# Kernel optimization log

Measured on AMD Instinct MI355X. Metric: run time of the kernel, lower is better.

Reference implementation:

```python
import jax, jax.numpy as jnp
import numpy as np

HEADS = 8
GROUPS = 32   # Group_cnt in the source
WIN = 16      # config.local_window_size


def _gn_nc(x, groups, eps):
    # group_norm on [N, C] (affine=False)
    N, C = x.shape
    xg = x.reshape(N, groups, C // groups)
    m = xg.mean(axis=2, keepdims=True)
    v = xg.var(axis=2, keepdims=True)
    return ((xg - m) / jnp.sqrt(v + eps)).reshape(N, C)


def _gn_nchw(x, groups, eps):
    # group_norm on [B, C, H, W] (affine=False)
    B, C, H, W = x.shape
    xg = x.reshape(B, groups, C // groups, H, W)
    m = xg.mean(axis=(2, 3, 4), keepdims=True)
    v = xg.var(axis=(2, 3, 4), keepdims=True)
    return ((xg - m) / jnp.sqrt(v + eps)).reshape(B, C, H, W)


def _conv3x3(x, w, b=None):
    y = jax.lax.conv_general_dilated(x, w, (1, 1), 'SAME',
                                     dimension_numbers=('NCHW', 'OIHW', 'NCHW'))
    return y if b is None else y + b[None, :, None, None]


def _forward(x, temb, conv1_w, conv1_b, conv2_w, g_diff, g_res, g2, g3,
             qkv2_w, qkv2_b, out2_w, qkv3_w, qkv3_b, out3_w,
             lsa_qkv_w, lsa_out_w):
    # ---- Residual_Block (layer1) ----
    h = _gn_nchw(x, GROUPS, 1e-6)
    h = _conv3x3(h, conv1_w, conv1_b)
    h = h + g_diff * temb[:, :, None, None]      # gate_diffusion (ReZero-style gate)
    h = jax.nn.silu(h)
    h = _gn_nchw(h, GROUPS, 1e-6)
    h = _conv3x3(h, conv2_w)
    h = _gn_nchw(h, GROUPS, 1e-6)
    x = x + g_res * h                            # gate_residual

    B, C, Fq, T = x.shape
    Dh = C // HEADS
    scale = 1.0 / jnp.sqrt(jnp.float32(Dh))      # (F/heads)**0.5 divisor

    # ---- SelfAttention over frequency axis (layer2): batch B*T, seq Fq ----
    xf = x.transpose(0, 3, 2, 1).reshape(B * T, Fq, C)
    qkv = xf @ qkv2_w + qkv2_b                   # [B*T, Fq, 3C]
    q, k, v = [t.reshape(B * T, Fq, HEADS, Dh) for t in jnp.split(qkv, 3, axis=-1)]
    p = jax.nn.softmax(jnp.einsum('bLhf,blhf->bLlh', q, k) * scale, axis=2)
    y = jnp.einsum('blhf,bLlh->bLhf', v, p).reshape(B * T, Fq, C) @ out2_w
    y = _gn_nc(y.reshape(-1, C), GROUPS, 1e-5).reshape(B * T, Fq, C)
    xf = xf + g2 * y                             # gate2

    # ---- GlobalAttention over time axis (layer3): batch B*Fq, seq T ----
    xt = xf.reshape(B, T, Fq, C).transpose(0, 2, 1, 3).reshape(B * Fq, T, C)
    qkv = xt @ qkv3_w + qkv3_b
    q, k, v = [t.reshape(B * Fq, T, HEADS, Dh) for t in jnp.split(qkv, 3, axis=-1)]
    p = jax.nn.softmax(jnp.einsum('bhf,blhf->blh', q.mean(axis=1), k) * scale, axis=1)
    y = jnp.einsum('blhf,blh->bhf', v, p).reshape(B * Fq, C) @ out3_w
    y = _gn_nc(y, GROUPS, 1e-5).reshape(B * Fq, 1, C)
    xt = xt + g3 * y                             # gate3, broadcast over T
    x = xt.reshape(B, Fq, T, C).transpose(0, 3, 1, 2)

    # ---- LSA_block (layer4): pre-norm local windowed attention along T, residual ----
    h = _gn_nchw(x, GROUPS, 1e-5)
    h = h.transpose(0, 2, 3, 1).reshape(B * Fq, T, C)
    nw = T // WIN
    qkv = (h @ lsa_qkv_w).reshape(B * Fq, nw, WIN, 3 * C)
    q, k, v = [t.reshape(B * Fq, nw, WIN, HEADS, Dh) for t in jnp.split(qkv, 3, axis=-1)]
    p = jax.nn.softmax(jnp.einsum('nwqhd,nwkhd->nwqkh', q, k) * scale, axis=3)
    o = jnp.einsum('nwqkh,nwkhd->nwqhd', p, v).reshape(B * Fq, T, C) @ lsa_out_w
    return x + o.reshape(B, Fq, T, C).transpose(0, 3, 1, 2)


def setup_inputs() -> dict:
    key = jax.random.key(0)
    ks = jax.random.split(key, 10)
    B, C, Fq, T = 4, 256, 64, 256
    w = lambda k, s: jax.random.normal(k, s, dtype=jnp.float32) * 0.02
    return {
        'x': jax.random.normal(ks[0], (B, C, Fq, T), dtype=jnp.float32),
        'temb': jax.random.normal(ks[1], (B, C), dtype=jnp.float32),
        'conv1_w': w(ks[2], (C, C, 3, 3)),
        'conv1_b': jnp.zeros((C,), jnp.float32),
        'conv2_w': w(ks[3], (C, C, 3, 3)),
        'g_diff': jnp.full((1,), 0.5, jnp.float32),
        'g_res': jnp.full((1,), 0.5, jnp.float32),
        'g2': jnp.full((1,), 0.5, jnp.float32),
        'g3': jnp.full((1,), 0.5, jnp.float32),
        'qkv2_w': w(ks[4], (C, 3 * C)),
        'qkv2_b': jnp.zeros((3 * C,), jnp.float32),
        'out2_w': w(ks[5], (C, C)),
        'qkv3_w': w(ks[6], (C, 3 * C)),
        'qkv3_b': jnp.zeros((3 * C,), jnp.float32),
        'out3_w': w(ks[7], (C, C)),
        'lsa_qkv_w': w(ks[8], (C, 3 * C)),
        'lsa_out_w': w(ks[9], (C, C)),
    }


def reference(x, temb, conv1_w, conv1_b, conv2_w, g_diff, g_res, g2, g3,
              qkv2_w, qkv2_b, out2_w, qkv3_w, qkv3_b, out3_w,
              lsa_qkv_w, lsa_out_w):
    return _forward(x, temb, conv1_w, conv1_b, conv2_w, g_diff, g_res, g2, g3,
                    qkv2_w, qkv2_b, out2_w, qkv3_w, qkv3_b, out3_w,
                    lsa_qkv_w, lsa_out_w)
```

## Files before the change

### kernel.cpp

```cpp
#include <hip/hip_runtime.h>

#define NN 16777216
#define CC 256
#define FF 64
#define TT 256

typedef short v8s __attribute__((ext_vector_type(8)));
typedef float v4f __attribute__((ext_vector_type(4)));

__device__ __forceinline__ unsigned short f2bf(float f) {
  unsigned u = __float_as_uint(f);
  u += 0x7fff + ((u >> 16) & 1);
  return (unsigned short)(u >> 16);
}
__device__ __forceinline__ float bf2f(unsigned short h) {
  return __uint_as_float(((unsigned)h) << 16);
}
__device__ __forceinline__ unsigned packbf2(float a, float b) {
  return (unsigned)f2bf(a) | ((unsigned)f2bf(b) << 16);
}
__device__ __forceinline__ void unpack8(uint4 u, float* d) {
  d[0] = __uint_as_float(u.x << 16); d[1] = __uint_as_float(u.x & 0xffff0000u);
  d[2] = __uint_as_float(u.y << 16); d[3] = __uint_as_float(u.y & 0xffff0000u);
  d[4] = __uint_as_float(u.z << 16); d[5] = __uint_as_float(u.z & 0xffff0000u);
  d[6] = __uint_as_float(u.w << 16); d[7] = __uint_as_float(u.w & 0xffff0000u);
}

__device__ __forceinline__ void blockReduce2(float& a, float& b, float* sbuf) {
  #pragma unroll
  for (int off = 32; off > 0; off >>= 1) {
    a += __shfl_down(a, off, 64);
    b += __shfl_down(b, off, 64);
  }
  int w = threadIdx.x >> 6;
  if ((threadIdx.x & 63) == 0) { sbuf[w] = a; sbuf[4 + w] = b; }
  __syncthreads();
  if (threadIdx.x == 0) {
    a = sbuf[0] + sbuf[1] + sbuf[2] + sbuf[3];
    b = sbuf[4] + sbuf[5] + sbuf[6] + sbuf[7];
  }
}

__global__ void prep_all_k(const float* __restrict__ c1w, const float* __restrict__ c2w,
    const float* __restrict__ q2w, const float* __restrict__ o2w, const float* __restrict__ q3w,
    const float* __restrict__ lqw, const float* __restrict__ low,
    unsigned short* __restrict__ WB1, unsigned short* __restrict__ WB2,
    unsigned short* __restrict__ Q2T, unsigned short* __restrict__ O2T,
    unsigned short* __restrict__ Q3T, unsigned short* __restrict__ LQT,
    unsigned short* __restrict__ LOT, float* __restrict__ stats) {
  long s = (long)blockIdx.x * 256 + threadIdx.x;
  if (s < 1024) { stats[s] = 0.f; return; }
  s -= 1024;
  if (s < 589824) {
    int co = (int)(s / 2304), r = (int)(s % 2304);
    int ci = r / 9, tap = r % 9;
    WB1[(tap * 256 + co) * 256 + ci] = f2bf(c1w[s]);
    return;
  }
  s -= 589824;
  if (s < 589824) {
    int co = (int)(s / 2304), r = (int)(s % 2304);
    int ci = r / 9, tap = r % 9;
    WB2[(tap * 256 + co) * 256 + ci] = f2bf(c2w[s]);
    return;
  }
  s -= 589824;
  if (s < 196608) { int k = (int)(s / 768), n = (int)(s % 768); Q2T[n * 256 + k] = f2bf(q2w[s]); return; }
  s -= 196608;
  if (s < 65536)  { int k = (int)(s / 256), n = (int)(s % 256); O2T[n * 256 + k] = f2bf(o2w[s]); return; }
  s -= 65536;
  if (s < 196608) { int k = (int)(s / 768), n = (int)(s % 768); Q3T[n * 256 + k] = f2bf(q3w[s]); return; }
  s -= 196608;
  if (s < 196608) { int k = (int)(s / 768), n = (int)(s % 768); LQT[n * 256 + k] = f2bf(lqw[s]); return; }
  s -= 196608;
  if (s < 65536)  { int k = (int)(s / 256), n = (int)(s % 256); LOT[n * 256 + k] = f2bf(low[s]); return; }
}

__global__ __launch_bounds__(256) void gn_stats_contig(const float* __restrict__ src, float* __restrict__ stats) {
  __shared__ float sbuf[8];
  int grp = blockIdx.x >> 3, chunk = blockIdx.x & 7;
  const float4* p = (const float4*)src + grp * 32768 + chunk * 4096;
  float s = 0.f, ss = 0.f;
  for (int i = threadIdx.x; i < 4096; i += 256) {
    float4 v = p[i];
    s += v.x + v.y + v.z + v.w;
    ss += v.x * v.x + v.y * v.y + v.z * v.z + v.w * v.w;
  }
  blockReduce2(s, ss, sbuf);
  if (threadIdx.x == 0) { atomicAdd(&stats[grp], s); atomicAdd(&stats[128 + grp], ss); }
}

__global__ __launch_bounds__(256) void gn_apply_tr_k(const float* __restrict__ src,
    const float* __restrict__ stats, unsigned short* __restrict__ XC, float eps) {
  __shared__ float sT[32][33];
  int bx = blockIdx.x;
  int r = bx >> 6;
  int c0 = ((bx >> 3) & 7) * 32;
  int t0 = (bx & 7) * 32;
  int b = r >> 6, f = r & 63;
  int tl = threadIdx.x & 31, tr = threadIdx.x >> 5;
  #pragma unroll
  for (int i = 0; i < 4; ++i) {
    int c = c0 + tr + i * 8;
    int grp = b * 32 + (c >> 3);
    float mean = stats[grp] * (1.f / 131072.f);
    float var = stats[128 + grp] * (1.f / 131072.f) - mean * mean;
    float rv = rsqrtf(var + eps);
    float v = src[((b * 256 + c) * 64 + f) * 256 + t0 + tl];
    sT[tr + i * 8][tl] = (v - mean) * rv;
  }
  __syncthreads();
  #pragma unroll
  for (int i = 0; i < 4; ++i) {
    int t = t0 + tr + i * 8;
    XC[(((size_t)(b * 64 + f)) * 256 + t) * 256 + c0 + tl] = f2bf(sT[tl][tr + i * 8]);
  }
}

__global__ __launch_bounds__(256) void gn_tr_resid_k(const float* __restrict__ h,
    const float* __restrict__ x, const float* __restrict__ stats,
    const float* __restrict__ gate, float* __restrict__ XF, float eps) {
  __shared__ float sT[32][33];
  int bx = blockIdx.x;
  int r = bx >> 6;
  int c0 = ((bx >> 3) & 7) * 32;
  int t0 = (bx & 7) * 32;
  int b = r >> 6, f = r & 63;
  int tl = threadIdx.x & 31, tr = threadIdx.x >> 5;
  float g = gate[0];
  #pragma unroll
  for (int i = 0; i < 4; ++i) {
    int c = c0 + tr + i * 8;
    int grp = b * 32 + (c >> 3);
    float mean = stats[grp] * (1.f / 131072.f);
    float var = stats[128 + grp] * (1.f / 131072.f) - mean * mean;
    float rv = rsqrtf(var + eps);
    int idx = ((b * 256 + c) * 64 + f) * 256 + t0 + tl;
    sT[tr + i * 8][tl] = x[idx] + g * (h[idx] - mean) * rv;
  }
  __syncthreads();
  #pragma unroll
  for (int i = 0; i < 4; ++i) {
    int t = t0 + tr + i * 8;
    XF[(((size_t)(b * 256 + t)) * 64 + f) * 256 + c0 + tl] = sT[tl][tr + i * 8];
  }
}

__global__ __launch_bounds__(256, 4) void conv3x3_mfma_k(const unsigned short* __restrict__ XC,
    const unsigned short* __restrict__ wb, const float* __restrict__ bias,
    const float* __restrict__ temb, const float* __restrict__ gd,
    float* __restrict__ out, float* __restrict__ ostats, int mode) {
  __shared__ __align__(16) unsigned short sIn[258][40];
  __shared__ __align__(16) unsigned short sW[3][64][40];
  int f  = blockIdx.x;
  int b  = blockIdx.y >> 2;
  int co0 = (blockIdx.y & 3) * 64;
  int tid = threadIdx.x;
  int wave = tid >> 6, lane = tid & 63;
  int lm = lane & 15, quad = lane >> 4;
  int w64 = wave * 64;
  v4f acc[4][4];
  #pragma unroll
  for (int i = 0; i < 4; ++i)
    #pragma unroll
    for (int j = 0; j < 4; ++j) acc[i][j] = (v4f)(0.f);

  for (int ci0 = 0; ci0 < 256; ci0 += 32) {
    for (int df = 0; df < 3; ++df) {
      __syncthreads();
      for (int s = tid; s < 1032; s += 256) {
        int tl = s >> 2, part = s & 3;
        int fi = f + df - 1, tg = tl - 1;
        uint4 val = make_uint4(0, 0, 0, 0);
        if (fi >= 0 && fi < 64 && tg >= 0 && tg < 256)
          val = *(const uint4*)&XC[(((size_t)(b * 64 + fi)) * 256 + tg) * 256 + ci0 + part * 8];
        *(uint4*)&sIn[tl][part * 8] = val;
      }
      for (int s = tid; s < 768; s += 256) {
        int tap3 = s >> 8, r = s & 255;
        int co = r >> 2, part = r & 3;
        *(uint4*)&sW[tap3][co][part * 8] =
            *(const uint4*)&wb[((size_t)((df * 3 + tap3) * 256) + co0 + co) * 256 + ci0 + part * 8];
      }
      __syncthreads();
      #pragma unroll
      for (int dt = 0; dt < 3; ++dt) {
        v8s A[4];
        #pragma unroll
        for (int mt = 0; mt < 4; ++mt)
          A[mt] = *(const v8s*)&sIn[w64 + mt * 16 + lm + dt][quad * 8];
        #pragma unroll
        for (int nt = 0; nt < 4; ++nt) {
          v8s B = *(const v8s*)&sW[dt][nt * 16 + lm][quad * 8];
          #pragma unroll
          for (int mt = 0; mt < 4; ++mt)
            acc[mt][nt] = __builtin_amdgcn_mfma_f32_16x16x32_bf16(A[mt], B, acc[mt][nt], 0, 0, 0);
        }
      }
    }
  }
  __syncthreads();
  float* sStat = (float*)sIn;
  float gdv = mode ? gd[0] : 0.f;
  float sch, qch;
  #pragma unroll
  for (int nt = 0; nt < 4; ++nt) {
    int co = co0 + nt * 16 + lm;
    float bb = 0.f;
    if (mode) bb = bias[co] + gdv * temb[b * 256 + co];
    sch = 0.f; qch = 0.f;
    #pragma unroll
    for (int mt = 0; mt < 4; ++mt) {
      int t = w64 + mt * 16 + quad * 4;
      float v0 = acc[mt][nt][0] + bb, v1 = acc[mt][nt][1] + bb;
      float v2 = acc[mt][nt][2] + bb, v3 = acc[mt][nt][3] + bb;
      if (mode) {
        v0 = v0 / (1.f + expf(-v0)); v1 = v1 / (1.f + expf(-v1));
        v2 = v2 / (1.f + expf(-v2)); v3 = v3 / (1.f + expf(-v3));
      }
      float4 o; o.x = v0; o.y = v1; o.z = v2; o.w = v3;
      *(float4*)&out[(((size_t)b * 256 + co) * 64 + f) * 256 + t] = o;
      sch += v0 + v1 + v2 + v3;
      qch += v0 * v0 + v1 * v1 + v2 * v2 + v3 * v3;
    }
    sch += __shfl_xor(sch, 16); qch += __shfl_xor(qch, 16);
    sch += __shfl_xor(sch, 32); qch += __shfl_xor(qch, 32);
    if (quad == 0) {
      sStat[((wave * 4 + nt) * 16 + lm) * 2]     = sch;
      sStat[((wave * 4 + nt) * 16 + lm) * 2 + 1] = qch;
    }
  }
  __syncthreads();
  if (tid < 64) {
    int c = tid;
    int nt = c >> 4, lmm = c & 15;
    float s = 0.f, q = 0.f;
    #pragma unroll
    for (int w = 0; w < 4; ++w) {
      s += sStat[((w * 4 + nt) * 16 + lmm) * 2];
      q += sStat[((w * 4 + nt) * 16 + lmm) * 2 + 1];
    }
    s += __shfl_xor(s, 1); q += __shfl_xor(q, 1);
    s += __shfl_xor(s, 2); q += __shfl_xor(q, 2);
    s += __shfl_xor(s, 4); q += __shfl_xor(q, 4);
    if ((c & 7) == 0) {
      int g = (co0 + c) >> 3;
      atomicAdd(&ostats[b * 32 + g], s);
      atomicAdd(&ostats[128 + b * 32 + g], q);
    }
  }
}

__global__ __launch_bounds__(256) void gemm_af32_k(const float* __restrict__ A, int lda,
    const unsigned short* __restrict__ BT, const float* __restrict__ bias,
    unsigned short* __restrict__ Cb, int ldc,
    const float* __restrict__ gstats, int growbase, float eps) {
  __shared__ __align__(16) unsigned short sA[128][40];
  __shared__ __align__(16) unsigned short sB[128][40];
  int n0 = blockIdx.x * 128, m0 = blockIdx.y * 128;
  int tid = threadIdx.x;
  int wave = tid >> 6, lane = tid & 63;
  int wm = wave >> 1, wn = wave & 1;
  int lm = lane & 15, quad = lane >> 4;
  v4f acc[4][4];
  #pragma unroll
  for (int i = 0; i < 4; ++i)
    #pragma unroll
    for (int j = 0; j < 4; ++j) acc[i][j] = (v4f)(0.f);

  for (int k0 = 0; k0 < 256; k0 += 32) {
    __syncthreads();
    #pragma unroll
    for (int i = 0; i < 4; ++i) {
      int s = tid + i * 256;
      int row = s >> 3, k4 = s & 7;
      float4 av = *(const float4*)&A[(size_t)(m0 + row) * lda + k0 + k4 * 4];
      if (gstats) {
        int grp = ((growbase + m0 + row) >> 14) * 32 + ((k0 + k4 * 4) >> 3);
        float mean = gstats[grp] * (1.f / 131072.f);
        float var = gstats[128 + grp] * (1.f / 131072.f) - mean * mean;
        float rr = rsqrtf(var + eps);
        av.x = (av.x - mean) * rr; av.y = (av.y - mean) * rr;
        av.z = (av.z - mean) * rr; av.w = (av.w - mean) * rr;
      }
      *(uint2*)&sA[row][k4 * 4] = make_uint2(packbf2(av.x, av.y), packbf2(av.z, av.w));
    }
    #pragma unroll
    for (int i = 0; i < 2; ++i) {
      int s = tid + i * 256;
      int n = s >> 2, part = s & 3;
      *(uint4*)&sB[n][part * 8] = *(const uint4*)&BT[(size_t)(n0 + n) * 256 + k0 + part * 8];
    }
    __syncthreads();
    v8s Af[4];
    #pragma unroll
    for (int mt = 0; mt < 4; ++mt)
      Af[mt] = *(const v8s*)&sA[wm * 64 + mt * 16 + lm][quad * 8];
    #pragma unroll
    for (int nt = 0; nt < 4; ++nt) {
      v8s Bf = *(const v8s*)&sB[wn * 64 + nt * 16 + lm][quad * 8];
      #pragma unroll
      for (int mt = 0; mt < 4; ++mt)
        acc[mt][nt] = __builtin_amdgcn_mfma_f32_16x16x32_bf16(Af[mt], Bf, acc[mt][nt], 0, 0, 0);
    }
  }
  #pragma unroll
  for (int nt = 0; nt < 4; ++nt) {
    int col = n0 + wn * 64 + nt * 16 + lm;
    float bb = bias ? bias[col] : 0.f;
    #pragma unroll
    for (int mt = 0; mt < 4; ++mt) {
      int row = m0 + wm * 64 + mt * 16 + quad * 4;
      #pragma unroll
      for (int r = 0; r < 4; ++r)
        Cb[(size_t)(row + r) * ldc + col] = f2bf(acc[mt][nt][r] + bb);
    }
  }
}

__global__ __launch_bounds__(256) void gemm_abf16_k(const unsigned short* __restrict__ A, int lda,
    const unsigned short* __restrict__ BT, float* __restrict__ xf,
    unsigned short* __restrict__ Cb, int ldc, const float* __restrict__ gate) {
  __shared__ __align__(16) unsigned short sA[128][40];
  __shared__ __align__(16) unsigned short sB[128][40];
  int n0 = blockIdx.x * 128, m0 = blockIdx.y * 128;
  int tid = threadIdx.x;
  int wave = tid >> 6, lane = tid & 63;
  int wm = wave >> 1, wn = wave & 1;
  int lm = lane & 15, quad = lane >> 4;
  v4f acc[4][4];
  #pragma unroll
  for (int i = 0; i < 4; ++i)
    #pragma unroll
    for (int j = 0; j < 4; ++j) acc[i][j] = (v4f)(0.f);

  for (int k0 = 0; k0 < 256; k0 += 32) {
    __syncthreads();
    #pragma unroll
    for (int i = 0; i < 2; ++i) {
      int s = tid + i * 256;
      int row = s >> 2, part = s & 3;
      *(uint4*)&sA[row][part * 8] = *(const uint4*)&A[(size_t)(m0 + row) * lda + k0 + part * 8];
      *(uint4*)&sB[row][part * 8] = *(const uint4*)&BT[(size_t)(n0 + row) * 256 + k0 + part * 8];
    }
    __syncthreads();
    v8s Af[4];
    #pragma unroll
    for (int mt = 0; mt < 4; ++mt)
      Af[mt] = *(const v8s*)&sA[wm * 64 + mt * 16 + lm][quad * 8];
    #pragma unroll
    for (int nt = 0; nt < 4; ++nt) {
      v8s Bf = *(const v8s*)&sB[wn * 64 + nt * 16 + lm][quad * 8];
      #pragma unroll
      for (int mt = 0; mt < 4; ++mt)
        acc[mt][nt] = __builtin_amdgcn_mfma_f32_16x16x32_bf16(Af[mt], Bf, acc[mt][nt], 0, 0, 0);
    }
  }
  if (xf) {
    float g = gate[0];
    #pragma unroll
    for (int mt = 0; mt < 4; ++mt) {
      int rowb = m0 + wm * 64 + mt * 16 + quad * 4;
      #pragma unroll
      for (int r = 0; r < 4; ++r) {
        #pragma unroll
        for (int nt = 0; nt < 4; ++nt) {
          float v = acc[mt][nt][r];
          float s = v, q = v * v;
          s += __shfl_xor(s, 1); q += __shfl_xor(q, 1);
          s += __shfl_xor(s, 2); q += __shfl_xor(q, 2);
          s += __shfl_xor(s, 4); q += __shfl_xor(q, 4);
          float m = s * 0.125f;
          float var = q * 0.125f - m * m;
          float norm = (v - m) * rsqrtf(var + 1e-5f);
          int col = n0 + wn * 64 + nt * 16 + lm;
          size_t idx = (size_t)(rowb + r) * 256 + col;
          xf[idx] += g * norm;
        }
      }
    }
  } else {
    #pragma unroll
    for (int nt = 0; nt < 4; ++nt) {
      int col = n0 + wn * 64 + nt * 16 + lm;
      #pragma unroll
      for (int mt = 0; mt < 4; ++mt) {
        int row = m0 + wm * 64 + mt * 16 + quad * 4;
        #pragma unroll
        for (int r = 0; r < 4; ++r)
          Cb[(size_t)(row + r) * ldc + col] = f2bf(acc[mt][nt][r]);
      }
    }
  }
}

__global__ __launch_bounds__(256) void gemm_k(const float* __restrict__ A, int lda,
    const float* __restrict__ Bm, int N, const float* __restrict__ bias,
    float* __restrict__ Cm, int ldc) {
  __shared__ __align__(16) float sA[16][64];
  __shared__ __align__(16) float sB[16][64];
  int n0 = blockIdx.x * 64, m0 = blockIdx.y * 64;
  int tid = threadIdx.x;
  int tx = tid & 15, ty = tid >> 4;
  int arow = m0 + (tid >> 2), acol = (tid & 3) * 4;
  int brow = tid >> 4, bcol = (tid & 15) * 4;
  float acc[4][4] = {};
  for (int k0 = 0; k0 < 256; k0 += 16) {
    __syncthreads();
    float4 av = *(const float4*)&A[(size_t)arow * lda + k0 + acol];
    sA[acol + 0][tid >> 2] = av.x;
    sA[acol + 1][tid >> 2] = av.y;
    sA[acol + 2][tid >> 2] = av.z;
    sA[acol + 3][tid >> 2] = av.w;
    *(float4*)&sB[brow][bcol] = *(const float4*)&Bm[(k0 + brow) * N + n0 + bcol];
    __syncthreads();
    #pragma unroll
    for (int kk = 0; kk < 16; ++kk) {
      float4 a = *(const float4*)&sA[kk][ty * 4];
      float4 b = *(const float4*)&sB[kk][tx * 4];
      float aa[4] = {a.x, a.y, a.z, a.w};
      float bb[4] = {b.x, b.y, b.z, b.w};
      #pragma unroll
      for (int i = 0; i < 4; ++i)
        #pragma unroll
        for (int j = 0; j < 4; ++j)
          acc[i][j] += aa[i] * bb[j];
    }
  }
  #pragma unroll
  for (int i = 0; i < 4; ++i)
    #pragma unroll
    for (int j = 0; j < 4; ++j) {
      int n = n0 + tx * 4 + j;
      float v = acc[i][j];
      if (bias) v += bias[n];
      Cm[(size_t)(m0 + ty * 4 + i) * ldc + n] = v;
    }
}

__global__ __launch_bounds__(256) void xf_to_xt_k(const float* __restrict__ XF, float* __restrict__ XT) {
  int rowid = blockIdx.x * 4 + (threadIdx.x >> 6);
  int lane = threadIdx.x & 63;
  int b = rowid >> 14, f = (rowid >> 8) & 63, t = rowid & 255;
  int src = ((b * TT + t) * FF + f) * CC + lane * 4;
  int dst = rowid * CC + lane * 4;
  *(float4*)&XT[dst] = *(const float4*)&XF[src];
}

__global__ __launch_bounds__(256) void final_out_k(const float* __restrict__ XT,
    const unsigned short* __restrict__ O2b, float* __restrict__ out, int rbase) {
  __shared__ float sT[32][33];
  int bx = blockIdx.x;
  int rl = bx >> 6;
  int t0 = ((bx >> 3) & 7) * 32;
  int c0 = (bx & 7) * 32;
  int rg = rbase + rl;
  int b = rg >> 6, f = rg & 63;
  int tc = threadIdx.x & 31, tr = threadIdx.x >> 5;
  #pragma unroll
  for (int i = 0; i < 4; ++i) {
    int t = t0 + tr + i * 8;
    sT[tr + i * 8][tc] = XT[(size_t)rg * 65536 + t * 256 + c0 + tc]
                       + bf2f(O2b[(size_t)rl * 65536 + t * 256 + c0 + tc]);
  }
  __syncthreads();
  #pragma unroll
  for (int i = 0; i < 4; ++i) {
    int c = c0 + tr + i * 8;
    out[((b * CC + c) * FF + f) * TT + t0 + tc] = sT[tc][tr + i * 8];
  }
}

__global__ __launch_bounds__(256) void attn2_mfma_k(unsigned short* __restrict__ Q) {
  __shared__ __align__(16) unsigned short sP[4][64][72];
  __shared__ __align__(16) unsigned short sVt[4][32][72];
  int bt = blockIdx.x;
  int tid = threadIdx.x;
  int wave = tid >> 6, lane = tid & 63;
  int lm = lane & 15, quad = lane >> 4;
  const float scale = 0.17677669529663687f;
  size_t rowbase = (size_t)bt * 64;
  unsigned short (*P)[72] = sP[wave];
  unsigned short (*Vt)[72] = sVt[wave];
  #pragma unroll
  for (int hh = 0; hh < 2; ++hh) {
    int h = wave * 2 + hh;
    int hoff = h * 32;
    v8s Af[4], Bf[4];
    #pragma unroll
    for (int mt = 0; mt < 4; ++mt)
      Af[mt] = *(const v8s*)&Q[(rowbase + mt * 16 + lm) * 768 + hoff + quad * 8];
    #pragma unroll
    for (int nt = 0; nt < 4; ++nt)
      Bf[nt] = *(const v8s*)&Q[(rowbase + nt * 16 + lm) * 768 + 256 + hoff + quad * 8];
    v4f S[4][4];
    #pragma unroll
    for (int mt = 0; mt < 4; ++mt)
      #pragma unroll
      for (int nt = 0; nt < 4; ++nt)
        S[mt][nt] = __builtin_amdgcn_mfma_f32_16x16x32_bf16(Af[mt], Bf[nt], (v4f)(0.f), 0, 0, 0);
    #pragma unroll
    for (int part = 0; part < 4; ++part) {
      uint4 u = *(const uint4*)&Q[(rowbase + lane) * 768 + 512 + hoff + part * 8];
      unsigned short* up = (unsigned short*)&u;
      #pragma unroll
      for (int j = 0; j < 8; ++j) Vt[part * 8 + j][lane] = up[j];
    }
    float inv[4][4];
    #pragma unroll
    for (int mt = 0; mt < 4; ++mt) {
      #pragma unroll
      for (int r = 0; r < 4; ++r) {
        float v0 = S[mt][0][r] * scale, v1 = S[mt][1][r] * scale;
        float v2 = S[mt][2][r] * scale, v3 = S[mt][3][r] * scale;
        float mx = fmaxf(fmaxf(v0, v1), fmaxf(v2, v3));
        mx = fmaxf(mx, __shfl_xor(mx, 1));
        mx = fmaxf(mx, __shfl_xor(mx, 2));
        mx = fmaxf(mx, __shfl_xor(mx, 4));
        mx = fmaxf(mx, __shfl_xor(mx, 8));
        float e0 = __expf(v0 - mx), e1 = __expf(v1 - mx);
        float e2 = __expf(v2 - mx), e3 = __expf(v3 - mx);
        float sm = e0 + e1 + e2 + e3;
        sm += __shfl_xor(sm, 1);
        sm += __shfl_xor(sm, 2);
        sm += __shfl_xor(sm, 4);
        sm += __shfl_xor(sm, 8);
        inv[mt][r] = 1.f / sm;
        int row = mt * 16 + quad * 4 + r;
        P[row][lm]      = f2bf(e0);
        P[row][16 + lm] = f2bf(e1);
        P[row][32 + lm] = f2bf(e2);
        P[row][48 + lm] = f2bf(e3);
      }
    }
    v8s Ap[4][2], Bv[2][2];
    #pragma unroll
    for (int mt = 0; mt < 4; ++mt)
      #pragma unroll
      for (int kc = 0; kc < 2; ++kc)
        Ap[mt][kc] = *(const v8s*)&P[mt * 16 + lm][kc * 32 + quad * 8];
    #pragma unroll
    for (int nd = 0; nd < 2; ++nd)
      #pragma unroll
      for (int kc = 0; kc < 2; ++kc)
        Bv[nd][kc] = *(const v8s*)&Vt[nd * 16 + lm][kc * 32 + quad * 8];
    #pragma unroll
    for (int mt = 0; mt < 4; ++mt) {
      #pragma unroll
      for (int nd = 0; nd < 2; ++nd) {
        v4f O = (v4f)(0.f);
        O = __builtin_amdgcn_mfma_f32_16x16x32_bf16(Ap[mt][0], Bv[nd][0], O, 0, 0, 0);
        O = __builtin_amdgcn_mfma_f32_16x16x32_bf16(Ap[mt][1], Bv[nd][1], O, 0, 0, 0);
        #pragma unroll
        for (int r = 0; r < 4; ++r)
          P[mt * 16 + quad * 4 + r][nd * 16 + lm] = f2bf(O[r] * inv[mt][r]);
      }
    }
    #pragma unroll
    for (int part = 0; part < 4; ++part) {
      uint4 u = *(const uint4*)&P[lane][part * 8];
      *(uint4*)&Q[(rowbase + lane) * 768 + hoff + part * 8] = u;
    }
  }
}

__global__ __launch_bounds__(256) void attn3_k(const unsigned short* __restrict__ Q3,
                                               float* __restrict__ y3, int bf_base) {
  __shared__ float sQp[64][33];
  __shared__ float sqm[32];
  __shared__ float sp[256];
  __shared__ float sred[256];
  int bfl = blockIdx.x >> 3, h = blockIdx.x & 7;
  int tid = threadIdx.x;
  int tq = tid >> 2, c4 = tid & 3;
  int d8 = c4 * 8;
  const float scale = 0.17677669529663687f;
  size_t rowbase = (size_t)bfl * 256;
  {
    float a[8] = {};
    #pragma unroll
    for (int i = 0; i < 4; ++i) {
      int t = i * 64 + tq;
      float v[8];
      unpack8(*(const uint4*)&Q3[(rowbase + t) * 768 + h * 32 + d8], v);
      #pragma unroll
      for (int j = 0; j < 8; ++j) a[j] += v[j];
    }
    #pragma unroll
    for (int j = 0; j < 8; ++j) sQp[tq][d8 + j] = a[j];
  }
  __syncthreads();
  if (tid < 32) {
    float m = 0.f;
    for (int g = 0; g < 64; ++g) m += sQp[g][tid];
    sqm[tid] = m * (1.f / 256.f);
  }
  __syncthreads();
  {
    float dot = 0.f;
    #pragma unroll
    for (int p = 0; p < 4; ++p) {
      float v[8];
      unpack8(*(const uint4*)&Q3[(rowbase + tid) * 768 + 256 + h * 32 + p * 8], v);
      #pragma unroll
      for (int j = 0; j < 8; ++j) dot += sqm[p * 8 + j] * v[j];
    }
    sp[tid] = dot * scale;
    sred[tid] = sp[tid];
  }
  __syncthreads();
  for (int st = 128; st > 0; st >>= 1) { if (tid < st) sred[tid] = fmaxf(sred[tid], sred[tid + st]); __syncthreads(); }
  float mx = sred[0];
  __syncthreads();
  float e = expf(sp[tid] - mx);
  sred[tid] = e;
  __syncthreads();
  for (int st = 128; st > 0; st >>= 1) { if (tid < st) sred[tid] += sred[tid + st]; __syncthreads(); }
  float rinv = 1.f / sred[0];
  sp[tid] = e * rinv;
  __syncthreads();
  {
    float a[8] = {};
    #pragma unroll
    for (int i = 0; i < 4; ++i) {
      int t = i * 64 + tq;
      float w = sp[t];
      float v[8];
      unpack8(*(const uint4*)&Q3[(rowbase + t) * 768 + 512 + h * 32 + d8], v);
      #pragma unroll
      for (int j = 0; j < 8; ++j) a[j] += w * v[j];
    }
    #pragma unroll
    for (int j = 0; j < 8; ++j) sQp[tq][d8 + j] = a[j];
  }
  __syncthreads();
  if (tid < 32) {
    float o = 0.f;
    for (int g = 0; g < 64; ++g) o += sQp[g][tid];
    y3[(size_t)(bf_base + bfl) * 256 + h * 32 + tid] = o;
  }
}

__global__ __launch_bounds__(256) void lsa_attn_k(unsigned short* __restrict__ Q4) {
  __shared__ __align__(16) float sX[16][772];
  __shared__ float sS[8][16][17];
  __shared__ float sInv[8][16];
  int bfl = blockIdx.x >> 4, w = blockIdx.x & 15;
  int tid = threadIdx.x;
  size_t rb = ((size_t)(bfl * 256 + w * 16)) * 768;
  for (int s = tid; s < 1536; s += 256) {
    int t = s / 96, c8 = (s - t * 96) * 8;
    unpack8(*(const uint4*)&Q4[rb + t * 768 + c8], &sX[t][c8]);
  }
  __syncthreads();
  const float scale = 0.17677669529663687f;
  #pragma unroll
  for (int rep = 0; rep < 8; ++rep) {
    int idx = tid + rep * 256;
    int h = idx >> 8, q = (idx >> 4) & 15, k = idx & 15;
    float dot = 0.f;
    const float* qp = &sX[q][h * 32];
    const float* kp = &sX[k][256 + h * 32];
    for (int d = 0; d < 32; ++d) dot += qp[d] * kp[d];
    sS[h][q][k] = dot * scale;
  }
  __syncthreads();
  if (tid < 128) {
    int h = tid >> 4, q = tid & 15;
    float mx = -1e30f;
    for (int k = 0; k < 16; ++k) mx = fmaxf(mx, sS[h][q][k]);
    float sum = 0.f;
    for (int k = 0; k < 16; ++k) { float e = expf(sS[h][q][k] - mx); sS[h][q][k] = e; sum += e; }
    sInv[h][q] = 1.f / sum;
  }
  __syncthreads();
  #pragma unroll
  for (int rep = 0; rep < 8; ++rep) {
    int idx = tid + rep * 256;
    int t = idx >> 7, c2 = (idx & 127) * 2;
    int h = c2 >> 5;
    float a0 = 0.f, a1 = 0.f;
    for (int k = 0; k < 16; ++k) {
      float p = sS[h][t][k];
      a0 += p * sX[k][512 + c2];
      a1 += p * sX[k][512 + c2 + 1];
    }
    float riv = sInv[h][t];
    *(unsigned*)&Q4[rb + t * 768 + c2] = packbf2(a0 * riv, a1 * riv);
  }
}

__global__ void gn_rows_k(const float* __restrict__ src, float* __restrict__ dst, int total) {
  int s = blockIdx.x * 256 + threadIdx.x;
  if (s >= total) return;
  int base = s * 8;
  float4 a = *(const float4*)&src[base];
  float4 b = *(const float4*)&src[base + 4];
  float m = (a.x + a.y + a.z + a.w + b.x + b.y + b.z + b.w) * 0.125f;
  float q = (a.x * a.x + a.y * a.y + a.z * a.z + a.w * a.w +
             b.x * b.x + b.y * b.y + b.z * b.z + b.w * b.w) * 0.125f - m * m;
  float r = rsqrtf(q + 1e-5f);
  a.x = (a.x - m) * r; a.y = (a.y - m) * r; a.z = (a.z - m) * r; a.w = (a.w - m) * r;
  b.x = (b.x - m) * r; b.y = (b.y - m) * r; b.z = (b.z - m) * r; b.w = (b.w - m) * r;
  *(float4*)&dst[base] = a;
  *(float4*)&dst[base + 4] = b;
}

__global__ __launch_bounds__(256) void bcast_add_k(float* __restrict__ XT, const float* __restrict__ y3n,
                                                   const float* __restrict__ gate) {
  int i4 = blockIdx.x * 256 + threadIdx.x;
  int flat = i4 * 4;
  int r = flat >> 16, c = flat & 255;
  float g = gate[0];
  float4 v = ((float4*)XT)[i4];
  float4 a = *(const float4*)&y3n[r * 256 + c];
  v.x += g * a.x; v.y += g * a.y; v.z += g * a.z; v.w += g * a.w;
  ((float4*)XT)[i4] = v;
}

__global__ __launch_bounds__(256) void gn_stats_xt_k(const float* __restrict__ X, float* __restrict__ stats) {
  __shared__ float sbuf[8];
  int bx = blockIdx.x;
  int b = bx >> 11, g = (bx >> 6) & 31, f = bx & 63;
  size_t base = (size_t)(b * 64 + f) * 65536 + g * 8;
  float s = 0.f, ss = 0.f;
  for (int i = threadIdx.x; i < 2048; i += 256) {
    int t = i >> 3, c = i & 7;
    float v = X[base + t * 256 + c];
    s += v; ss += v * v;
  }
  blockReduce2(s, ss, sbuf);
  if (threadIdx.x == 0) { atomicAdd(&stats[b * 32 + g], s); atomicAdd(&stats[128 + b * 32 + g], ss); }
}

extern "C" void kernel_launch(void* const* d_in, const int* in_sizes, int n_in,
                              void* d_out, int out_size, void* d_ws, size_t ws_size,
                              hipStream_t stream) {
  (void)in_sizes; (void)n_in; (void)out_size;
  const float* x        = (const float*)d_in[0];
  const float* temb     = (const float*)d_in[1];
  const float* conv1_w  = (const float*)d_in[2];
  const float* conv1_b  = (const float*)d_in[3];
  const float* conv2_w  = (const float*)d_in[4];
  const float* g_diff   = (const float*)d_in[5];
  const float* g_res    = (const float*)d_in[6];
  const float* g2       = (const float*)d_in[7];
  const float* g3       = (const float*)d_in[8];
  const float* qkv2_w   = (const float*)d_in[9];
  const float* qkv2_b   = (const float*)d_in[10];
  const float* out2_w   = (const float*)d_in[11];
  const float* qkv3_w   = (const float*)d_in[12];
  const float* qkv3_b   = (const float*)d_in[13];
  const float* out3_w   = (const float*)d_in[14];
  const float* lsa_qkv_w = (const float*)d_in[15];
  const float* lsa_out_w = (const float*)d_in[16];
  float* out = (float*)d_out;
  float* ws = (float*)d_ws;

  int NCHv = 4;
  {
    auto need = [](int nch) -> size_t {
      size_t rows = 65536 / nch;
      size_t uslots = rows * 512;
      if (uslots < 8388608) uslots = 8388608;
      return 4ull * ((size_t)NN + uslots + 950272 + 198000);
    };
    if (ws_size >= need(1)) NCHv = 1;
    else if (ws_size >= need(2)) NCHv = 2;
  }
  const size_t rows = 65536 / NCHv;

  float* W = ws;
  float* U = ws + (size_t)NN;
  unsigned short* XC  = (unsigned short*)U;
  unsigned short* QB  = (unsigned short*)U;
  unsigned short* O2B = (unsigned short*)(U + rows * 384);
  size_t uslots = rows * 512; if (uslots < 8388608) uslots = 8388608;
  float* WREG = U + uslots;
  unsigned short* WB1   = (unsigned short*)WREG;
  unsigned short* WB2   = WB1 + 589824;
  unsigned short* QKV2T = WB2 + 589824;
  unsigned short* OUT2T = QKV2T + 196608;
  unsigned short* QKV3T = OUT2T + 65536;
  unsigned short* LSAQT = QKV3T + 196608;
  unsigned short* LSAOT = LSAQT + 196608;
  float* Y3    = WREG + 950272;
  float* Y3O   = Y3 + 65536;
  float* Y3N   = Y3O + 65536;
  float* STATS = Y3N + 65536;
  float* ST0 = STATS, *ST1 = STATS + 256, *ST2 = STATS + 512, *ST3 = STATS + 768;
  float* D = out;

  dim3 b256(256);
  prep_all_k<<<7428, b256, 0, stream>>>(conv1_w, conv2_w, qkv2_w, out2_w, qkv3_w,
                                        lsa_qkv_w, lsa_out_w,
                                        WB1, WB2, QKV2T, OUT2T, QKV3T, LSAQT, LSAOT, STATS);

  gn_stats_contig<<<1024, b256, 0, stream>>>(x, ST0);
  gn_apply_tr_k<<<16384, b256, 0, stream>>>(x, ST0, XC, 1e-6f);
  conv3x3_mfma_k<<<dim3(64, 16), b256, 0, stream>>>(XC, WB1, conv1_b, temb, g_diff, W, ST1, 1);
  gn_apply_tr_k<<<16384, b256, 0, stream>>>(W, ST1, XC, 1e-6f);
  conv3x3_mfma_k<<<dim3(64, 16), b256, 0, stream>>>(XC, WB2, nullptr, nullptr, nullptr, W, ST2, 0);
  gn_tr_resid_k<<<16384, b256, 0, stream>>>(W, x, ST2, g_res, D, 1e-6f);

  for (int c = 0; c < NCHv; ++c) {
    float* XFr = D + (size_t)c * rows * 256;
    gemm_af32_k<<<dim3(6, rows / 128), b256, 0, stream>>>(XFr, 256, QKV2T, qkv2_b, QB, 768, nullptr, 0, 0.f);
    attn2_mfma_k<<<rows / 64, b256, 0, stream>>>(QB);
    gemm_abf16_k<<<dim3(2, rows / 128), b256, 0, stream>>>(QB, 768, OUT2T, XFr, nullptr, 256, g2);
  }

  xf_to_xt_k<<<16384, b256, 0, stream>>>(D, W);
  for (int c = 0; c < NCHv; ++c) {
    const float* XTr = W + (size_t)c * rows * 256;
    gemm_af32_k<<<dim3(6, rows / 128), b256, 0, stream>>>(XTr, 256, QKV3T, qkv3_b, QB, 768, nullptr, 0, 0.f);
    attn3_k<<<(rows / 256) * 8, b256, 0, stream>>>(QB, Y3, c * (int)(rows / 256));
  }
  gemm_k<<<dim3(4, 4), b256, 0, stream>>>(Y3, 256, out3_w, 256, nullptr, Y3O, 256);
  gn_rows_k<<<32, b256, 0, stream>>>(Y3O, Y3N, 8192);
  bcast_add_k<<<16384, b256, 0, stream>>>(W, Y3N, g3);

  gn_stats_xt_k<<<8192, b256, 0, stream>>>(W, ST3);
  for (int c = 0; c < NCHv; ++c) {
    const float* XTr = W + (size_t)c * rows * 256;
    gemm_af32_k<<<dim3(6, rows / 128), b256, 0, stream>>>(XTr, 256, LSAQT, nullptr, QB, 768,
                                                          ST3, (int)(c * rows), 1e-5f);
    lsa_attn_k<<<(rows / 256) * 16, b256, 0, stream>>>(QB);
    gemm_abf16_k<<<dim3(2, rows / 128), b256, 0, stream>>>(QB, 768, LSAOT, nullptr, O2B, 256, nullptr);
    final_out_k<<<(rows / 256) * 64, b256, 0, stream>>>(W, O2B, out, c * (int)(rows / 256));
  }
}
```

Before: 1.057 ms.

## Fuse group-norm stats into broadcast add, GN into gemm epilogue, swizzle block order

```diff
diff --git a/kernel.cpp b/kernel.cpp
--- a/kernel.cpp
+++ b/kernel.cpp
@@ -152,9 +152,12 @@
     float* __restrict__ out, float* __restrict__ ostats, int mode) {
   __shared__ __align__(16) unsigned short sIn[258][40];
   __shared__ __align__(16) unsigned short sW[3][64][40];
-  int f  = blockIdx.x;
-  int b  = blockIdx.y >> 2;
-  int co0 = (blockIdx.y & 3) * 64;
+  int bid0 = blockIdx.y * 64 + blockIdx.x;
+  int nb = (bid0 & 7) * 128 + (bid0 >> 3);
+  int f  = nb & 63;
+  int yy = nb >> 6;
+  int b  = yy >> 2;
+  int co0 = (yy & 3) * 64;
   int tid = threadIdx.x;
   int wave = tid >> 6, lane = tid & 63;
   int lm = lane & 15, quad = lane >> 4;
@@ -257,7 +260,11 @@
     const float* __restrict__ gstats, int growbase, float eps) {
   __shared__ __align__(16) unsigned short sA[128][40];
   __shared__ __align__(16) unsigned short sB[128][40];
-  int n0 = blockIdx.x * 128, m0 = blockIdx.y * 128;
+  int nbx = gridDim.x;
+  int nwg = nbx * gridDim.y;
+  int bid0 = blockIdx.y * nbx + blockIdx.x;
+  int nb = (bid0 & 7) * (nwg >> 3) + (bid0 >> 3);
+  int n0 = (nb % nbx) * 128, m0 = (nb / nbx) * 128;
   int tid = threadIdx.x;
   int wave = tid >> 6, lane = tid & 63;
   int wm = wave >> 1, wn = wave & 1;
@@ -323,7 +330,11 @@
     unsigned short* __restrict__ Cb, int ldc, const float* __restrict__ gate) {
   __shared__ __align__(16) unsigned short sA[128][40];
   __shared__ __align__(16) unsigned short sB[128][40];
-  int n0 = blockIdx.x * 128, m0 = blockIdx.y * 128;
+  int nbx = gridDim.x;
+  int nwg = nbx * gridDim.y;
+  int bid0 = blockIdx.y * nbx + blockIdx.x;
+  int nb = (bid0 & 7) * (nwg >> 3) + (bid0 >> 3);
+  int n0 = (nb % nbx) * 128, m0 = (nb / nbx) * 128;
   int tid = threadIdx.x;
   int wave = tid >> 6, lane = tid & 63;
   int wm = wave >> 1, wn = wave & 1;
@@ -396,7 +407,7 @@
 
 __global__ __launch_bounds__(256) void gemm_k(const float* __restrict__ A, int lda,
     const float* __restrict__ Bm, int N, const float* __restrict__ bias,
-    float* __restrict__ Cm, int ldc) {
+    float* __restrict__ Cm, int ldc, int gn) {
   __shared__ __align__(16) float sA[16][64];
   __shared__ __align__(16) float sB[16][64];
   int n0 = blockIdx.x * 64, m0 = blockIdx.y * 64;
@@ -428,14 +439,26 @@
     }
   }
   #pragma unroll
-  for (int i = 0; i < 4; ++i)
+  for (int i = 0; i < 4; ++i) {
+    float m = 0.f, rv = 1.f;
+    if (gn) {
+      float s = acc[i][0] + acc[i][1] + acc[i][2] + acc[i][3];
+      float q = acc[i][0] * acc[i][0] + acc[i][1] * acc[i][1]
+              + acc[i][2] * acc[i][2] + acc[i][3] * acc[i][3];
+      s += __shfl_xor(s, 1); q += __shfl_xor(q, 1);
+      m = s * 0.125f;
+      float var = q * 0.125f - m * m;
+      rv = rsqrtf(var + 1e-5f);
+    }
     #pragma unroll
     for (int j = 0; j < 4; ++j) {
       int n = n0 + tx * 4 + j;
       float v = acc[i][j];
-      if (bias) v += bias[n];
+      if (gn) v = (v - m) * rv;
+      else if (bias) v += bias[n];
       Cm[(size_t)(m0 + ty * 4 + i) * ldc + n] = v;
     }
+  }
 }
 
 __global__ __launch_bounds__(256) void xf_to_xt_k(const float* __restrict__ XF, float* __restrict__ XT) {
@@ -690,25 +713,13 @@
   }
 }
 
-__global__ void gn_rows_k(const float* __restrict__ src, float* __restrict__ dst, int total) {
-  int s = blockIdx.x * 256 + threadIdx.x;
-  if (s >= total) return;
-  int base = s * 8;
-  float4 a = *(const float4*)&src[base];
-  float4 b = *(const float4*)&src[base + 4];
-  float m = (a.x + a.y + a.z + a.w + b.x + b.y + b.z + b.w) * 0.125f;
-  float q = (a.x * a.x + a.y * a.y + a.z * a.z + a.w * a.w +
-             b.x * b.x + b.y * b.y + b.z * b.z + b.w * b.w) * 0.125f - m * m;
-  float r = rsqrtf(q + 1e-5f);
-  a.x = (a.x - m) * r; a.y = (a.y - m) * r; a.z = (a.z - m) * r; a.w = (a.w - m) * r;
-  b.x = (b.x - m) * r; b.y = (b.y - m) * r; b.z = (b.z - m) * r; b.w = (b.w - m) * r;
-  *(float4*)&dst[base] = a;
-  *(float4*)&dst[base + 4] = b;
-}
-
 __global__ __launch_bounds__(256) void bcast_add_k(float* __restrict__ XT, const float* __restrict__ y3n,
-                                                   const float* __restrict__ gate) {
-  int i4 = blockIdx.x * 256 + threadIdx.x;
+                                                   const float* __restrict__ gate, float* __restrict__ stats) {
+  __shared__ float sacc[64];
+  int tid = threadIdx.x;
+  if (tid < 64) sacc[tid] = 0.f;
+  __syncthreads();
+  int i4 = blockIdx.x * 256 + tid;
   int flat = i4 * 4;
   int r = flat >> 16, c = flat & 255;
   float g = gate[0];
@@ -716,21 +727,20 @@
   float4 a = *(const float4*)&y3n[r * 256 + c];
   v.x += g * a.x; v.y += g * a.y; v.z += g * a.z; v.w += g * a.w;
   ((float4*)XT)[i4] = v;
-}
-
-__global__ __launch_bounds__(256) void gn_stats_xt_k(const float* __restrict__ X, float* __restrict__ stats) {
-  __shared__ float sbuf[8];
-  int bx = blockIdx.x;
-  int b = bx >> 11, g = (bx >> 6) & 31, f = bx & 63;
-  size_t base = (size_t)(b * 64 + f) * 65536 + g * 8;
-  float s = 0.f, ss = 0.f;
-  for (int i = threadIdx.x; i < 2048; i += 256) {
-    int t = i >> 3, c = i & 7;
-    float v = X[base + t * 256 + c];
-    s += v; ss += v * v;
-  }
-  blockReduce2(s, ss, sbuf);
-  if (threadIdx.x == 0) { atomicAdd(&stats[b * 32 + g], s); atomicAdd(&stats[128 + b * 32 + g], ss); }
+  float s = v.x + v.y + v.z + v.w;
+  float q = v.x * v.x + v.y * v.y + v.z * v.z + v.w * v.w;
+  s += __shfl_xor(s, 1); q += __shfl_xor(q, 1);
+  if ((tid & 1) == 0) {
+    int grp = (c >> 3) & 31;
+    atomicAdd(&sacc[grp * 2], s);
+    atomicAdd(&sacc[grp * 2 + 1], q);
+  }
+  __syncthreads();
+  if (tid < 32) {
+    int b = blockIdx.x >> 12;
+    atomicAdd(&stats[b * 32 + tid], sacc[tid * 2]);
+    atomicAdd(&stats[128 + b * 32 + tid], sacc[tid * 2 + 1]);
+  }
 }
 
 extern "C" void kernel_launch(void* const* d_in, const int* in_sizes, int n_in,
@@ -816,11 +826,9 @@
     gemm_af32_k<<<dim3(6, rows / 128), b256, 0, stream>>>(XTr, 256, QKV3T, qkv3_b, QB, 768, nullptr, 0, 0.f);
     attn3_k<<<(rows / 256) * 8, b256, 0, stream>>>(QB, Y3, c * (int)(rows / 256));
   }
-  gemm_k<<<dim3(4, 4), b256, 0, stream>>>(Y3, 256, out3_w, 256, nullptr, Y3O, 256);
-  gn_rows_k<<<32, b256, 0, stream>>>(Y3O, Y3N, 8192);
-  bcast_add_k<<<16384, b256, 0, stream>>>(W, Y3N, g3);
-
-  gn_stats_xt_k<<<8192, b256, 0, stream>>>(W, ST3);
+  gemm_k<<<dim3(4, 4), b256, 0, stream>>>(Y3, 256, out3_w, 256, nullptr, Y3N, 256, 1);
+  bcast_add_k<<<16384, b256, 0, stream>>>(W, Y3N, g3, ST3);
+
   for (int c = 0; c < NCHv; ++c) {
     const float* XTr = W + (size_t)c * rows * 256;
     gemm_af32_k<<<dim3(6, rows / 128), b256, 0, stream>>>(XTr, 256, LSAQT, nullptr, QB, 768,
```

New measurement: 1.087 ms. 1.03x slower.
